# Performance work log

Measured on AMD Instinct MI355X. Metric: run time of the kernel, lower is better.

The kernel has to match this reference:

```python
import jax, jax.numpy as jnp
import numpy as np

B, IN_DIM, D, N, OUT_DIM, H = 8192, 512, 512, 16, 1024, 4

def setup_inputs() -> dict:
    key = jax.random.key(0)
    ks = jax.random.split(key, 20)
    s = lambda *sh: 0.02
    def w(k, *sh):
        return jax.random.normal(k, sh, dtype=jnp.float32) * 0.02
    return {
        "x": jax.random.normal(ks[0], (B, IN_DIM), dtype=jnp.float32),
        "W_in": w(ks[1], D, IN_DIM), "b_in": jnp.zeros((D,), jnp.float32),
        "init_states": jax.random.normal(ks[2], (1, N, D), dtype=jnp.float32),
        "Wz": w(ks[3], D, 2 * D), "bz": jnp.zeros((D,), jnp.float32),
        "Wr": w(ks[4], D, 2 * D), "br": jnp.zeros((D,), jnp.float32),
        "Wh": w(ks[5], D, 2 * D), "bh": jnp.zeros((D,), jnp.float32),
        "Wqkv": w(ks[6], 3 * D, D), "bqkv": jnp.zeros((3 * D,), jnp.float32),
        "Wo": w(ks[7], D, D), "bo": jnp.zeros((D,), jnp.float32),
        "Wg": w(ks[8], D, 2 * D), "bg": jnp.zeros((D,), jnp.float32),
        "W_out": w(ks[9], OUT_DIM, N * D), "b_out": jnp.zeros((OUT_DIM,), jnp.float32),
    }

def _forward(x, W_in, b_in, init_states, Wz, bz, Wr, br, Wh, bh,
             Wqkv, bqkv, Wo, bo, Wg, bg, W_out, b_out):
    b = x.shape[0]
    xp = x @ W_in.T + b_in                                  # [B, D]
    inp = jnp.broadcast_to(xp[:, None, :], (b, N, D))       # repeat across state nodes
    s = jnp.broadcast_to(init_states, (b, N, D))            # [B, N, D]

    # ---- GRU-style gated update per state node ----
    comb = jnp.concatenate([s, inp], axis=-1)               # [B, N, 2D]
    z = jax.nn.sigmoid(comb @ Wz.T + bz)
    r = jax.nn.sigmoid(comb @ Wr.T + br)
    cand = jnp.tanh(jnp.concatenate([r * s, inp], axis=-1) @ Wh.T + bh)
    s = (1.0 - z) * s + z * cand                            # [B, N, D]

    # ---- inter-state communication: multihead self-attention over N nodes ----
    dh = D // H
    qkv = s @ Wqkv.T + bqkv                                 # [B, N, 3D]
    q, k, v = jnp.split(qkv, 3, axis=-1)
    q = q.reshape(b, N, H, dh)
    k = k.reshape(b, N, H, dh)
    v = v.reshape(b, N, H, dh)
    scores = jnp.einsum('bnhd,bmhd->bhnm', q, k) / jnp.sqrt(jnp.float32(dh))
    attn = jax.nn.softmax(scores, axis=-1)
    ctx = jnp.einsum('bhnm,bmhd->bnhd', attn, v).reshape(b, N, D)
    ctx = ctx @ Wo.T + bo                                   # [B, N, D]

    # gated mix of own state and communicated state
    g = jax.nn.sigmoid(jnp.concatenate([s, ctx], axis=-1) @ Wg.T + bg)
    s = g * s + (1.0 - g) * ctx                             # [B, N, D]

    pooled = s.reshape(b, N * D)
    return pooled @ W_out.T + b_out                          # [B, OUT_DIM]

def reference(x, W_in, b_in, init_states, Wz, bz, Wr, br, Wh, bh,
              Wqkv, bqkv, Wo, bo, Wg, bg, W_out, b_out):
    return _forward(x, W_in, b_in, init_states, Wz, bz, Wr, br, Wh, bh,
                    Wqkv, bqkv, Wo, bo, Wg, bg, W_out, b_out)
```

## Files before the change

kernel.cpp:

```cpp
#include <hip/hip_runtime.h>

typedef __bf16 bf16;
typedef __attribute__((ext_vector_type(8))) __bf16 bf16x8;
typedef __attribute__((ext_vector_type(4))) __bf16 bf16x4;
typedef __attribute__((ext_vector_type(2))) __bf16 bf16x2;
typedef __attribute__((ext_vector_type(4))) float f32x4;

#define BM 128
#define BN 128
#define BK 64

__device__ __forceinline__ void async_cp16(const bf16* g, bf16* l) {
    __builtin_amdgcn_global_load_lds((const __attribute__((address_space(1))) void*)g,
                                     (__attribute__((address_space(3))) void*)l, 16, 0, 0);
}
__device__ __forceinline__ float sigm(float x) { return 1.0f / (1.0f + __expf(-x)); }

template<int EPI, bool DUAL>
__global__ __launch_bounds__(256, 2)
void gemm_bt(const bf16* __restrict__ A, const bf16* __restrict__ Bw,
             const bf16* __restrict__ A2, const bf16* __restrict__ B2,
             int M, int N, int K,
             float* __restrict__ outf, bf16* __restrict__ outb,
             const float* __restrict__ bias,
             const float* __restrict__ zrh, const float* __restrict__ bh,
             const float* __restrict__ bz,
             const float* __restrict__ zs, const float* __restrict__ S0,
             const bf16* __restrict__ s1p, const bf16* __restrict__ c2p)
{
    __shared__ bf16 As[BM * BK];
    __shared__ bf16 Bs[BN * BK];
    const int tid  = threadIdx.x;
    const int lane = tid & 63;
    const int wave = tid >> 6;
    const int wr = wave >> 1, wc = wave & 1;
    const size_t arow0 = (size_t)blockIdx.y * BM;
    const size_t brow0 = (size_t)blockIdx.x * BN;
    const int srow = tid >> 3;
    const int scol = (tid & 7) * 8;

    f32x4 acc[4][4];
    const f32x4 zero = {0.f, 0.f, 0.f, 0.f};
#pragma unroll
    for (int i = 0; i < 4; i++)
#pragma unroll
        for (int j = 0; j < 4; j++) acc[i][j] = zero;

    const int KT  = K / BK;
    const int TKT = DUAL ? 2 * KT : KT;
    for (int kt = 0; kt < TKT; ++kt) {
        const bf16* Ag; const bf16* Bg; int k0;
        if (!DUAL || kt < KT) { Ag = A;  Bg = Bw; k0 = kt * BK; }
        else                  { Ag = A2; Bg = B2; k0 = (kt - KT) * BK; }
        const bf16* ga = Ag + (arow0 + srow) * (size_t)K + k0 + scol;
        const bf16* gb = Bg + (brow0 + srow) * (size_t)K + k0 + scol;
        __syncthreads();
#pragma unroll
        for (int i = 0; i < 4; i++) {
            async_cp16(ga + (size_t)(i * 32) * K, As + wave * 512 + i * 2048);
            async_cp16(gb + (size_t)(i * 32) * K, Bs + wave * 512 + i * 2048);
        }
        __syncthreads();
        const bf16* Ab = As + (wr * 64 + (lane & 15)) * BK + ((lane >> 4) * 8);
        const bf16* Bb = Bs + (wc * 64 + (lane & 15)) * BK + ((lane >> 4) * 8);
#pragma unroll
        for (int kk = 0; kk < BK; kk += 32) {
            bf16x8 av[4], bv[4];
#pragma unroll
            for (int i = 0; i < 4; i++) {
                av[i] = *(const bf16x8*)(Ab + i * 16 * BK + kk);
                bv[i] = *(const bf16x8*)(Bb + i * 16 * BK + kk);
            }
#pragma unroll
            for (int mi = 0; mi < 4; mi++)
#pragma unroll
                for (int ni = 0; ni < 4; ni++)
                    acc[mi][ni] = __builtin_amdgcn_mfma_f32_16x16x32_bf16(av[mi], bv[ni], acc[mi][ni], 0, 0, 0);
        }
    }

    const int mbase = (int)arow0 + wr * 64;
    const int nbase = (int)brow0 + wc * 64;
#pragma unroll
    for (int mi = 0; mi < 4; mi++) {
#pragma unroll
        for (int ni = 0; ni < 4; ni++) {
            f32x4 v = acc[mi][ni];
            const int n  = nbase + ni * 16 + (lane & 15);
            const int m0 = mbase + mi * 16 + (lane >> 4) * 4;
#pragma unroll
            for (int r = 0; r < 4; r++) {
                const int m = m0 + r;
                const float val = v[r];
                const size_t oidx = (size_t)m * N + n;
                if constexpr (EPI == 0) {
                    outf[oidx] = val;
                } else if constexpr (EPI == 1) {
                    outb[oidx] = (bf16)(val + bias[n]);
                } else if constexpr (EPI == 2) {
                    const int brow_ = m >> 4, node = m & 15;
                    const float cand = tanhf(val + zrh[(size_t)brow_ * 1536 + 1024 + n] + bh[n]);
                    const float z = sigm(zrh[(size_t)brow_ * 1536 + n] + zs[node * 512 + n] + bz[n]);
                    const float s0v = S0[node * 512 + n];
                    outb[oidx] = (bf16)((1.f - z) * s0v + z * cand);
                } else if constexpr (EPI == 4) {
                    const float g = sigm(val + bias[n]);
                    outb[oidx] = (bf16)(g * (float)s1p[oidx] + (1.f - g) * (float)c2p[oidx]);
                } else {
                    outf[oidx] = val + bias[n];
                }
            }
        }
    }
}

__global__ __launch_bounds__(256)
void cvt_slice(bf16* __restrict__ dst, const float* __restrict__ src,
               int cols, int src_ld, int col0)
{
    const size_t i = ((size_t)blockIdx.x * 256 + threadIdx.x) * 4;
    const int r = (int)(i / cols), c = (int)(i % cols);
    float4 v = *(const float4*)(src + (size_t)r * src_ld + col0 + c);
    bf16x4 o; o[0] = (bf16)v.x; o[1] = (bf16)v.y; o[2] = (bf16)v.z; o[3] = (bf16)v.w;
    *(bf16x4*)(dst + i) = o;
}

__global__ __launch_bounds__(256)
void node_proj_kernel(const float* __restrict__ S0, const float* __restrict__ Wz,
                      const float* __restrict__ Wr, float* __restrict__ zs,
                      float* __restrict__ rs)
{
    alignas(16) __shared__ float srow[512];
    const int tid = threadIdx.x;
    const int which = blockIdx.x >> 4;
    const int n = blockIdx.x & 15;
    const float* W = which ? Wr : Wz;
    float* out = which ? rs : zs;
    for (int i = tid; i < 512; i += 256) srow[i] = S0[n * 512 + i];
    __syncthreads();
    for (int j = tid; j < 512; j += 256) {
        const float4* wrow = (const float4*)(W + (size_t)j * 1024);
        float acc = 0.f;
#pragma unroll 4
        for (int k = 0; k < 128; k++) {
            float4 wv = wrow[k];
            float4 sv = *(const float4*)(srow + k * 4);
            acc += sv.x * wv.x + sv.y * wv.y + sv.z * wv.z + sv.w * wv.w;
        }
        out[n * 512 + j] = acc;
    }
}

__global__ __launch_bounds__(256)
void gru_r_kernel(const float* __restrict__ zrh, const float* __restrict__ rs,
                  const float* __restrict__ br, const float* __restrict__ S0,
                  bf16* __restrict__ Ah)
{
    const size_t bn_ = blockIdx.x;
    const int b = (int)(bn_ >> 4), n = (int)(bn_ & 15);
    const int d = threadIdx.x * 2;
    const float2 rxv = *(const float2*)(zrh + (size_t)b * 1536 + 512 + d);
    const float2 rsv = *(const float2*)(rs + n * 512 + d);
    const float2 brv = *(const float2*)(br + d);
    const float2 s0v = *(const float2*)(S0 + n * 512 + d);
    bf16x2 o;
    o[0] = (bf16)(sigm(rxv.x + rsv.x + brv.x) * s0v.x);
    o[1] = (bf16)(sigm(rxv.y + rsv.y + brv.y) * s0v.y);
    *(bf16x2*)(Ah + bn_ * 512 + d) = o;
}

__global__ __launch_bounds__(256, 2)
void attn_kernel(const bf16* __restrict__ qkv, bf16* __restrict__ ctx)
{
    __shared__ bf16 sq[16 * 1544];
    __shared__ float attn_s[4][16][16];
    const int tid = threadIdx.x;
    const int lane = tid & 63, wave = tid >> 6;
    const size_t b = blockIdx.x;
    const bf16* src = qkv + b * 24576;
    for (int c = tid; c < 3072; c += 256) {
        int row = c / 192, col = c % 192;
        *(uint4*)(sq + row * 1544 + col * 8) = *(const uint4*)(src + (size_t)c * 8);
    }
    __syncthreads();
    const int h = wave;
#pragma unroll
    for (int t = 0; t < 4; t++) {
        int idx = t * 64 + lane;
        int i = idx >> 4, j = idx & 15;
        const bf16* qp = sq + i * 1544 + h * 128;
        const bf16* kp = sq + j * 1544 + 512 + h * 128;
        float s = 0.f;
#pragma unroll
        for (int k8 = 0; k8 < 128; k8 += 8) {
            bf16x8 qv = *(const bf16x8*)(qp + k8);
            bf16x8 kv = *(const bf16x8*)(kp + k8);
#pragma unroll
            for (int u = 0; u < 8; u++) s += (float)qv[u] * (float)kv[u];
        }
        attn_s[h][i][j] = s * 0.08838834764831845f;
    }
    __syncthreads();
    if (lane < 16) {
        float* row = &attn_s[h][lane][0];
        float mx = row[0];
#pragma unroll
        for (int j2 = 1; j2 < 16; j2++) mx = fmaxf(mx, row[j2]);
        float sum = 0.f;
#pragma unroll
        for (int j2 = 0; j2 < 16; j2++) { float pp = __expf(row[j2] - mx); row[j2] = pp; sum += pp; }
        float inv = 1.f / sum;
#pragma unroll
        for (int j2 = 0; j2 < 16; j2++) row[j2] *= inv;
    }
    __syncthreads();
    bf16* outp = ctx + b * 8192;
    for (int e = tid; e < 8192; e += 256) {
        int i = e >> 9, d = e & 511, h2 = d >> 7;
        float s = 0.f;
#pragma unroll
        for (int j2 = 0; j2 < 16; j2++) s += attn_s[h2][i][j2] * (float)sq[j2 * 1544 + 1024 + d];
        outp[i * 512 + d] = (bf16)s;
    }
}

extern "C" void kernel_launch(void* const* d_in, const int* in_sizes, int n_in,
                              void* d_out, int out_size, void* d_ws, size_t ws_size,
                              hipStream_t stream)
{
    (void)in_sizes; (void)n_in; (void)out_size;
    const float* x    = (const float*)d_in[0];
    const float* W_in = (const float*)d_in[1];
    const float* b_in = (const float*)d_in[2];
    const float* S0   = (const float*)d_in[3];
    const float* Wz   = (const float*)d_in[4];
    const float* bz   = (const float*)d_in[5];
    const float* Wr   = (const float*)d_in[6];
    const float* br   = (const float*)d_in[7];
    const float* Wh   = (const float*)d_in[8];
    const float* bh   = (const float*)d_in[9];
    const float* Wqkv = (const float*)d_in[10];
    const float* bqkv = (const float*)d_in[11];
    const float* Wo   = (const float*)d_in[12];
    const float* bo   = (const float*)d_in[13];
    const float* Wg   = (const float*)d_in[14];
    const float* bg   = (const float*)d_in[15];
    const float* Wout = (const float*)d_in[16];
    const float* bout = (const float*)d_in[17];
    float* out = (float*)d_out;
    char* p = (char*)d_ws;

    size_t off = 0;
    auto alloc = [&](size_t bytes) { size_t o = off; off += (bytes + 1023) & ~size_t(1023); return o; };
    const size_t o_s2      = alloc(131072ull * 512 * 2);
    const size_t o_xbf     = alloc(8192ull * 512 * 2);
    const size_t o_Win     = alloc(512ull * 512 * 2);
    const size_t o_W3x     = alloc(1536ull * 512 * 2);
    const size_t o_Whs     = alloc(512ull * 512 * 2);
    const size_t o_Wqkv    = alloc(1536ull * 512 * 2);
    const size_t o_Wo      = alloc(512ull * 512 * 2);
    const size_t o_Wgs     = alloc(512ull * 512 * 2);
    const size_t o_Wgc     = alloc(512ull * 512 * 2);
    const size_t o_Wout    = alloc(1024ull * 8192 * 2);
    const size_t o_zs      = alloc(16ull * 512 * 4);
    const size_t o_rs      = alloc(16ull * 512 * 4);
    const size_t fixed_end = off;

    const size_t per_c = 1024 + 6144 + 16384 + 16384 + 49152 + 16384 + 16384;
    int C = 0;
    for (int cand : {2048, 1024, 512, 256})
        if (fixed_end + (size_t)cand * per_c <= ws_size) { C = cand; break; }
    if (C == 0) return;

    const size_t o_xp   = fixed_end;
    const size_t o_zrh  = o_xp   + (size_t)C * 1024;
    const size_t o_Ah   = o_zrh  + (size_t)C * 6144;
    const size_t o_s1   = o_Ah   + (size_t)C * 16384;
    const size_t o_qkv  = o_s1   + (size_t)C * 16384;
    const size_t o_ctx  = o_qkv  + (size_t)C * 49152;
    const size_t o_ctx2 = o_ctx  + (size_t)C * 16384;

    bf16*  s2      = (bf16*)(p + o_s2);
    bf16*  x_bf    = (bf16*)(p + o_xbf);
    bf16*  Win_bf  = (bf16*)(p + o_Win);
    bf16*  W3x     = (bf16*)(p + o_W3x);
    bf16*  Whs     = (bf16*)(p + o_Whs);
    bf16*  Wqkv_bf = (bf16*)(p + o_Wqkv);
    bf16*  Wo_bf   = (bf16*)(p + o_Wo);
    bf16*  Wgs     = (bf16*)(p + o_Wgs);
    bf16*  Wgc     = (bf16*)(p + o_Wgc);
    bf16*  Wout_bf = (bf16*)(p + o_Wout);
    float* zs      = (float*)(p + o_zs);
    float* rs      = (float*)(p + o_rs);
    bf16*  xp_c    = (bf16*)(p + o_xp);
    float* zrh_c   = (float*)(p + o_zrh);
    bf16*  Ah_c    = (bf16*)(p + o_Ah);
    bf16*  s1_c    = (bf16*)(p + o_s1);
    bf16*  qkv_c   = (bf16*)(p + o_qkv);
    bf16*  ctx_c   = (bf16*)(p + o_ctx);
    bf16*  ctx2_c  = (bf16*)(p + o_ctx2);

    auto cvtl = [&](bf16* dst, const float* src, int rows, int cols, int ld, int c0) {
        cvt_slice<<<dim3(rows * cols / 1024), dim3(256), 0, stream>>>(dst, src, cols, ld, c0);
    };
    cvtl(x_bf, x, 8192, 512, 512, 0);
    cvtl(Win_bf, W_in, 512, 512, 512, 0);
    cvtl(W3x,              Wz, 512, 512, 1024, 512);
    cvtl(W3x + 512 * 512,  Wr, 512, 512, 1024, 512);
    cvtl(W3x + 1024 * 512, Wh, 512, 512, 1024, 512);
    cvtl(Whs, Wh, 512, 512, 1024, 0);
    cvtl(Wqkv_bf, Wqkv, 1536, 512, 512, 0);
    cvtl(Wo_bf, Wo, 512, 512, 512, 0);
    cvtl(Wgs, Wg, 512, 512, 1024, 0);
    cvtl(Wgc, Wg, 512, 512, 1024, 512);
    cvtl(Wout_bf, Wout, 1024, 8192, 8192, 0);
    node_proj_kernel<<<dim3(32), dim3(256), 0, stream>>>(S0, Wz, Wr, zs, rs);

    const int n_chunks = 8192 / C;
    for (int c = 0; c < n_chunks; ++c) {
        const size_t B0 = (size_t)c * C;
        const int Mc = C * 16;
        gemm_bt<1, false><<<dim3(4, C / 128), dim3(256), 0, stream>>>(
            x_bf + B0 * 512, Win_bf, nullptr, nullptr, C, 512, 512,
            nullptr, xp_c, b_in, nullptr, nullptr, nullptr, nullptr, nullptr, nullptr, nullptr);
        gemm_bt<0, false><<<dim3(12, C / 128), dim3(256), 0, stream>>>(
            xp_c, W3x, nullptr, nullptr, C, 1536, 512,
            zrh_c, nullptr, nullptr, nullptr, nullptr, nullptr, nullptr, nullptr, nullptr, nullptr);
        gru_r_kernel<<<dim3(C * 16), dim3(256), 0, stream>>>(zrh_c, rs, br, S0, Ah_c);
        gemm_bt<2, false><<<dim3(4, Mc / 128), dim3(256), 0, stream>>>(
            Ah_c, Whs, nullptr, nullptr, Mc, 512, 512,
            nullptr, s1_c, nullptr, zrh_c, bh, bz, zs, S0, nullptr, nullptr);
        gemm_bt<1, false><<<dim3(12, Mc / 128), dim3(256), 0, stream>>>(
            s1_c, Wqkv_bf, nullptr, nullptr, Mc, 1536, 512,
            nullptr, qkv_c, bqkv, nullptr, nullptr, nullptr, nullptr, nullptr, nullptr, nullptr);
        attn_kernel<<<dim3(C), dim3(256), 0, stream>>>(qkv_c, ctx_c);
        gemm_bt<1, false><<<dim3(4, Mc / 128), dim3(256), 0, stream>>>(
            ctx_c, Wo_bf, nullptr, nullptr, Mc, 512, 512,
            nullptr, ctx2_c, bo, nullptr, nullptr, nullptr, nullptr, nullptr, nullptr, nullptr);
        gemm_bt<4, true><<<dim3(4, Mc / 128), dim3(256), 0, stream>>>(
            s1_c, Wgs, ctx2_c, Wgc, Mc, 512, 512,
            nullptr, s2 + B0 * 8192, bg, nullptr, nullptr, nullptr, nullptr, nullptr, s1_c, ctx2_c);
    }
    gemm_bt<5, false><<<dim3(8, 64), dim3(256), 0, stream>>>(
        s2, Wout_bf, nullptr, nullptr, 8192, 1024, 8192,
        out, nullptr, bout, nullptr, nullptr, nullptr, nullptr, nullptr, nullptr, nullptr);
}
```

Baseline: 2.679 ms.

## Add 256x256 8-wave double-buffered GEMM with swizzled LDS and split-K output

Introduces a new GEMM kernel with 256x256 tiles, 8 waves, double-buffered LDS staging with XOR swizzle, interleaved async loads and MFMA phases with priority hints. It replaces the large per-node GEMMs and adds a split-K (2-way) atomic-add path for the final output projection, preceded by a zeroing kernel. The aim is higher data reuse and better overlap of global loads with MFMA. The costs are more register and LDS pressure, lower occupancy, extra atomics and nondeterministic summation order in the output.

```diff
diff --git a/kernel.cpp b/kernel.cpp
--- a/kernel.cpp
+++ b/kernel.cpp
@@ -6,27 +6,175 @@
 typedef __attribute__((ext_vector_type(2))) __bf16 bf16x2;
 typedef __attribute__((ext_vector_type(4))) float f32x4;
 
+__device__ __forceinline__ void async_cp16(const bf16* g, bf16* l) {
+    __builtin_amdgcn_global_load_lds((const __attribute__((address_space(1))) void*)g,
+                                     (__attribute__((address_space(3))) void*)l, 16, 0, 0);
+}
+__device__ __forceinline__ float sigm(float x) { return 1.0f / (1.0f + __expf(-x)); }
+
+#define BAR()  do { __builtin_amdgcn_s_barrier(); asm volatile("" ::: "memory"); } while (0)
+#define VMC4() asm volatile("s_waitcnt vmcnt(4)" ::: "memory")
+#define VMC0() asm volatile("s_waitcnt vmcnt(0)" ::: "memory")
+
+template<int EPI, bool DUAL, int SPLITK>
+__global__ __launch_bounds__(512, 2)
+void gemm8(const bf16* __restrict__ A, const bf16* __restrict__ Bw,
+           const bf16* __restrict__ A2, const bf16* __restrict__ B2,
+           int M, int N, int K,
+           float* __restrict__ outf, bf16* __restrict__ outb,
+           const float* __restrict__ bias,
+           const float* __restrict__ zrh, const float* __restrict__ bh,
+           const float* __restrict__ bz,
+           const float* __restrict__ zs, const float* __restrict__ S0,
+           const bf16* __restrict__ s1p, const bf16* __restrict__ c2p)
+{
+    __shared__ __align__(16) bf16 lds[2][2][16384];
+    const int tid  = threadIdx.x;
+    const int lane = tid & 63;
+    const int w    = tid >> 6;
+    const int wm   = w >> 2;
+    const int wn   = w & 3;
+    const size_t arow0 = (size_t)blockIdx.y * 256;
+    const size_t brow0 = (size_t)blockIdx.x * 256;
+
+    const int Ks  = K / SPLITK;
+    const int NT1 = Ks >> 6;
+    const int NTt = DUAL ? 2 * NT1 : NT1;
+    const bf16* Ap = A  + (size_t)blockIdx.z * Ks;
+    const bf16* Bp = Bw + (size_t)blockIdx.z * Ks;
+
+    const int rsub = w * 8 + (lane >> 3);
+    const int gcol = (((lane & 7) ^ (lane >> 3)) << 3);
+
+    auto stage = [&](int t, int mat, int h, int buf) {
+        if (t >= NTt) return;
+        const bf16* src; int k0;
+        if (!DUAL || t < NT1) { src = mat ? Bp : Ap; k0 = t << 6; }
+        else                  { src = mat ? B2 : A2; k0 = (t - NT1) << 6; }
+        const size_t rb = (mat ? brow0 : arow0) + (size_t)h * 128 + rsub;
+        const bf16* g = src + rb * (size_t)K + k0 + gcol;
+        bf16* d = &lds[buf][mat][(h * 128 + w * 8) * 64];
+        async_cp16(g, d);
+        async_cp16(g + (size_t)64 * K, d + 4096);
+    };
+
+    const int ar   = lane & 15;
+    const int klo  = (lane >> 4) << 4;
+    const int sxor = (lane & 7) << 4;
+
+    bf16x8 af[4][2];
+    bf16x8 bfr[4][2];
+    f32x4 acc[8][4];
+    const f32x4 zero = {0.f, 0.f, 0.f, 0.f};
+#pragma unroll
+    for (int i = 0; i < 8; i++)
+#pragma unroll
+        for (int j = 0; j < 4; j++) acc[i][j] = zero;
+
+    auto loadA = [&](int buf, int mh) {
+#pragma unroll
+        for (int mi = 0; mi < 4; mi++)
+#pragma unroll
+            for (int kk = 0; kk < 2; kk++) {
+                const int row = wm * 128 + mh * 64 + mi * 16 + ar;
+                const int cb  = (kk * 64 + klo) ^ sxor;
+                af[mi][kk] = *(const bf16x8*)((const char*)&lds[buf][0][0] + row * 128 + cb);
+            }
+    };
+    auto loadB = [&](int buf, int nlo) {
+#pragma unroll
+        for (int ni = 0; ni < 2; ni++)
+#pragma unroll
+            for (int kk = 0; kk < 2; kk++) {
+                const int row = wn * 64 + (nlo + ni) * 16 + ar;
+                const int cb  = (kk * 64 + klo) ^ sxor;
+                bfr[nlo + ni][kk] = *(const bf16x8*)((const char*)&lds[buf][1][0] + row * 128 + cb);
+            }
+    };
+    auto mm = [&](int mh, int nlo) {
+        __builtin_amdgcn_s_setprio(1);
+#pragma unroll
+        for (int mi = 0; mi < 4; mi++)
+#pragma unroll
+            for (int ni = 0; ni < 2; ni++) {
+                const int am = mh * 4 + mi, an = nlo + ni;
+                acc[am][an] = __builtin_amdgcn_mfma_f32_16x16x32_bf16(af[mi][0], bfr[an][0], acc[am][an], 0, 0, 0);
+                acc[am][an] = __builtin_amdgcn_mfma_f32_16x16x32_bf16(af[mi][1], bfr[an][1], acc[am][an], 0, 0, 0);
+            }
+        __builtin_amdgcn_s_setprio(0);
+    };
+
+    stage(0, 0, 0, 0); stage(0, 0, 1, 0); stage(0, 1, 0, 0); stage(0, 1, 1, 0);
+    stage(1, 1, 0, 1); stage(1, 1, 1, 1);
+    VMC4(); BAR();
+
+    for (int t = 0; t < NTt; t += 2) {
+        const int t2 = t + 2, t3 = t + 3;
+        loadA(0, 0); loadB(0, 0); stage(t + 1, 0, 0, 1);
+        BAR(); mm(0, 0); BAR();
+        loadB(0, 2); stage(t + 1, 0, 1, 1);
+        BAR(); mm(0, 2); BAR();
+        loadA(0, 1); stage(t2, 1, 0, 0);
+        BAR(); mm(1, 2); BAR();
+        stage(t2, 1, 1, 0);
+        if (t2 < NTt) { VMC4(); } else { VMC0(); }
+        BAR(); mm(1, 0); BAR();
+        loadA(1, 0); loadB(1, 0); stage(t2, 0, 0, 0);
+        BAR(); mm(0, 0); BAR();
+        loadB(1, 2); stage(t2, 0, 1, 0);
+        BAR(); mm(0, 2); BAR();
+        loadA(1, 1); stage(t3, 1, 0, 1);
+        BAR(); mm(1, 2); BAR();
+        stage(t3, 1, 1, 1);
+        if (t2 < NTt) { VMC4(); }
+        BAR(); mm(1, 0); BAR();
+    }
+
+#pragma unroll
+    for (int am = 0; am < 8; am++) {
+#pragma unroll
+        for (int an = 0; an < 4; an++) {
+            f32x4 v = acc[am][an];
+            const int n  = (int)brow0 + wn * 64 + an * 16 + (lane & 15);
+            const int m0 = (int)arow0 + wm * 128 + am * 16 + (lane >> 4) * 4;
+#pragma unroll
+            for (int r = 0; r < 4; r++) {
+                const int m = m0 + r;
+                const float val = v[r];
+                const size_t oidx = (size_t)m * N + n;
+                if constexpr (EPI == 1) {
+                    outb[oidx] = (bf16)(val + bias[n]);
+                } else if constexpr (EPI == 2) {
+                    const int brow_ = m >> 4;
+                    const int node = m & 15;
+                    const float cand = tanhf(val + zrh[(size_t)brow_ * 1536 + 1024 + n] + bh[n]);
+                    const float z = sigm(zrh[(size_t)brow_ * 1536 + n] + zs[node * 512 + n] + bz[n]);
+                    const float s0v = S0[node * 512 + n];
+                    outb[oidx] = (bf16)((1.f - z) * s0v + z * cand);
+                } else if constexpr (EPI == 4) {
+                    const float g = sigm(val + bias[n]);
+                    outb[oidx] = (bf16)(g * (float)s1p[oidx] + (1.f - g) * (float)c2p[oidx]);
+                } else {
+                    if constexpr (SPLITK > 1) {
+                        atomicAdd(&outf[oidx], val + (blockIdx.z == 0 ? bias[n] : 0.f));
+                    } else {
+                        outf[oidx] = val + bias[n];
+                    }
+                }
+            }
+        }
+    }
+}
+
 #define BM 128
 #define BN 128
 #define BK 64
-
-__device__ __forceinline__ void async_cp16(const bf16* g, bf16* l) {
-    __builtin_amdgcn_global_load_lds((const __attribute__((address_space(1))) void*)g,
-                                     (__attribute__((address_space(3))) void*)l, 16, 0, 0);
-}
-__device__ __forceinline__ float sigm(float x) { return 1.0f / (1.0f + __expf(-x)); }
-
-template<int EPI, bool DUAL>
+template<int EPI>
 __global__ __launch_bounds__(256, 2)
 void gemm_bt(const bf16* __restrict__ A, const bf16* __restrict__ Bw,
-             const bf16* __restrict__ A2, const bf16* __restrict__ B2,
              int M, int N, int K,
              float* __restrict__ outf, bf16* __restrict__ outb,
-             const float* __restrict__ bias,
-             const float* __restrict__ zrh, const float* __restrict__ bh,
-             const float* __restrict__ bz,
-             const float* __restrict__ zs, const float* __restrict__ S0,
-             const bf16* __restrict__ s1p, const bf16* __restrict__ c2p)
+             const float* __restrict__ bias)
 {
     __shared__ bf16 As[BM * BK];
     __shared__ bf16 Bs[BN * BK];
@@ -46,14 +194,11 @@
 #pragma unroll
         for (int j = 0; j < 4; j++) acc[i][j] = zero;
 
-    const int KT  = K / BK;
-    const int TKT = DUAL ? 2 * KT : KT;
-    for (int kt = 0; kt < TKT; ++kt) {
-        const bf16* Ag; const bf16* Bg; int k0;
-        if (!DUAL || kt < KT) { Ag = A;  Bg = Bw; k0 = kt * BK; }
-        else                  { Ag = A2; Bg = B2; k0 = (kt - KT) * BK; }
-        const bf16* ga = Ag + (arow0 + srow) * (size_t)K + k0 + scol;
-        const bf16* gb = Bg + (brow0 + srow) * (size_t)K + k0 + scol;
+    const int KT = K / BK;
+    for (int kt = 0; kt < KT; ++kt) {
+        const int k0 = kt * BK;
+        const bf16* ga = A  + (arow0 + srow) * (size_t)K + k0 + scol;
+        const bf16* gb = Bw + (brow0 + srow) * (size_t)K + k0 + scol;
         __syncthreads();
 #pragma unroll
         for (int i = 0; i < 4; i++) {
@@ -91,27 +236,20 @@
 #pragma unroll
             for (int r = 0; r < 4; r++) {
                 const int m = m0 + r;
-                const float val = v[r];
                 const size_t oidx = (size_t)m * N + n;
-                if constexpr (EPI == 0) {
-                    outf[oidx] = val;
-                } else if constexpr (EPI == 1) {
-                    outb[oidx] = (bf16)(val + bias[n]);
-                } else if constexpr (EPI == 2) {
-                    const int brow_ = m >> 4, node = m & 15;
-                    const float cand = tanhf(val + zrh[(size_t)brow_ * 1536 + 1024 + n] + bh[n]);
-                    const float z = sigm(zrh[(size_t)brow_ * 1536 + n] + zs[node * 512 + n] + bz[n]);
-                    const float s0v = S0[node * 512 + n];
-                    outb[oidx] = (bf16)((1.f - z) * s0v + z * cand);
-                } else if constexpr (EPI == 4) {
-                    const float g = sigm(val + bias[n]);
-                    outb[oidx] = (bf16)(g * (float)s1p[oidx] + (1.f - g) * (float)c2p[oidx]);
-                } else {
-                    outf[oidx] = val + bias[n];
-                }
-            }
-        }
-    }
+                if constexpr (EPI == 0) outf[oidx] = v[r];
+                else                    outb[oidx] = (bf16)(v[r] + bias[n]);
+            }
+        }
+    }
+}
+
+__global__ __launch_bounds__(256)
+void zero_f32(float* __restrict__ p)
+{
+    const size_t i = ((size_t)blockIdx.x * 256 + threadIdx.x) * 4;
+    float4 z; z.x = 0.f; z.y = 0.f; z.z = 0.f; z.w = 0.f;
+    *(float4*)(p + i) = z;
 }
 
 __global__ __launch_bounds__(256)
@@ -320,28 +458,27 @@
     for (int c = 0; c < n_chunks; ++c) {
         const size_t B0 = (size_t)c * C;
         const int Mc = C * 16;
-        gemm_bt<1, false><<<dim3(4, C / 128), dim3(256), 0, stream>>>(
-            x_bf + B0 * 512, Win_bf, nullptr, nullptr, C, 512, 512,
-            nullptr, xp_c, b_in, nullptr, nullptr, nullptr, nullptr, nullptr, nullptr, nullptr);
-        gemm_bt<0, false><<<dim3(12, C / 128), dim3(256), 0, stream>>>(
-            xp_c, W3x, nullptr, nullptr, C, 1536, 512,
-            zrh_c, nullptr, nullptr, nullptr, nullptr, nullptr, nullptr, nullptr, nullptr, nullptr);
+        gemm_bt<1><<<dim3(4, C / 128), dim3(256), 0, stream>>>(
+            x_bf + B0 * 512, Win_bf, C, 512, 512, nullptr, xp_c, b_in);
+        gemm_bt<0><<<dim3(12, C / 128), dim3(256), 0, stream>>>(
+            xp_c, W3x, C, 1536, 512, zrh_c, nullptr, nullptr);
         gru_r_kernel<<<dim3(C * 16), dim3(256), 0, stream>>>(zrh_c, rs, br, S0, Ah_c);
-        gemm_bt<2, false><<<dim3(4, Mc / 128), dim3(256), 0, stream>>>(
+        gemm8<2, false, 1><<<dim3(2, Mc / 256), dim3(512), 0, stream>>>(
             Ah_c, Whs, nullptr, nullptr, Mc, 512, 512,
             nullptr, s1_c, nullptr, zrh_c, bh, bz, zs, S0, nullptr, nullptr);
-        gemm_bt<1, false><<<dim3(12, Mc / 128), dim3(256), 0, stream>>>(
+        gemm8<1, false, 1><<<dim3(6, Mc / 256), dim3(512), 0, stream>>>(
             s1_c, Wqkv_bf, nullptr, nullptr, Mc, 1536, 512,
             nullptr, qkv_c, bqkv, nullptr, nullptr, nullptr, nullptr, nullptr, nullptr, nullptr);
         attn_kernel<<<dim3(C), dim3(256), 0, stream>>>(qkv_c, ctx_c);
-        gemm_bt<1, false><<<dim3(4, Mc / 128), dim3(256), 0, stream>>>(
+        gemm8<1, false, 1><<<dim3(2, Mc / 256), dim3(512), 0, stream>>>(
             ctx_c, Wo_bf, nullptr, nullptr, Mc, 512, 512,
             nullptr, ctx2_c, bo, nullptr, nullptr, nullptr, nullptr, nullptr, nullptr, nullptr);
-        gemm_bt<4, true><<<dim3(4, Mc / 128), dim3(256), 0, stream>>>(
+        gemm8<4, true, 1><<<dim3(2, Mc / 256), dim3(512), 0, stream>>>(
             s1_c, Wgs, ctx2_c, Wgc, Mc, 512, 512,
             nullptr, s2 + B0 * 8192, bg, nullptr, nullptr, nullptr, nullptr, nullptr, s1_c, ctx2_c);
     }
-    gemm_bt<5, false><<<dim3(8, 64), dim3(256), 0, stream>>>(
+    zero_f32<<<dim3(8192), dim3(256), 0, stream>>>(out);
+    gemm8<5, false, 2><<<dim3(4, 32, 2), dim3(512), 0, stream>>>(
         s2, Wout_bf, nullptr, nullptr, 8192, 1024, 8192,
         out, nullptr, bout, nullptr, nullptr, nullptr, nullptr, nullptr, nullptr, nullptr);
 }
```

New measurement: 3.373 ms. 25.9% more time.
